# Kernel tuning notes

Hardware: AMD Instinct MI355X
Metric: run time of the kernel (lower is better)

Reference implementation:

```python
import jax, jax.numpy as jnp
import numpy as np

N_NODES = 100000
N_EDGES = 1600000
IN_FEATS = 128
OUT_FEATS = 128
LN_EPS = 1e-5


def setup_inputs() -> dict:
    key = jax.random.key(0)
    k1, k2, k3, k4, k5 = jax.random.split(key, 5)
    h = jax.random.normal(k1, (N_NODES, IN_FEATS), dtype=jnp.float32)
    # nn.Linear(2*in_feats, out_feats): weight [out, 2*in], bias [out]
    stdv = 1.0 / np.sqrt(2 * IN_FEATS)
    W = jax.random.uniform(k2, (OUT_FEATS, 2 * IN_FEATS), dtype=jnp.float32, minval=-stdv, maxval=stdv)
    b = jax.random.uniform(k3, (OUT_FEATS,), dtype=jnp.float32, minval=-stdv, maxval=stdv)
    gamma = jnp.ones((OUT_FEATS,), dtype=jnp.float32)
    beta = jnp.zeros((OUT_FEATS,), dtype=jnp.float32)
    src = jax.random.randint(k4, (N_EDGES,), 0, N_NODES, dtype=jnp.int32)
    dst = jax.random.randint(k5, (N_EDGES,), 0, N_NODES, dtype=jnp.int32)
    return {"h": h, "W": W, "b": b, "gamma": gamma, "beta": beta, "src": src, "dst": dst}


def reference(h, W, b, gamma, beta, src, dst):
    n = h.shape[0]
    ones = jnp.ones(src.shape[0], dtype=h.dtype)
    deg = jax.ops.segment_sum(ones, dst, num_segments=n)          # in-degrees [N]
    norm = jnp.where(deg > 0, 1.0 / deg, 0.0)[:, None]            # inf -> 0
    ah = jax.ops.segment_sum(h[src], dst, num_segments=n)         # copy_src + sum: [N, D]
    cat = jnp.concatenate([h, ah * norm], axis=1)                 # [N, 2D]
    y = cat @ W.T + b                                             # linear -> [N, OUT]
    mu = jnp.mean(y, axis=-1, keepdims=True)
    var = jnp.mean((y - mu) ** 2, axis=-1, keepdims=True)
    y = (y - mu) * jax.lax.rsqrt(var + LN_EPS) * gamma + beta     # LayerNorm
    return jax.nn.relu(y)
```

## Files before the change

kernel.cpp:

```cpp
#include <hip/hip_runtime.h>
#include <hip/hip_bf16.h>

#define LN_EPS 1e-5f

#define NW 4096
#define CHUNK_CAP 96

#define CAP2 1280

#define S_MASK 0x1FFFFu

typedef __attribute__((ext_vector_type(8))) short short8;
typedef __attribute__((ext_vector_type(4))) float f32x4;
typedef __attribute__((ext_vector_type(2))) float f32x2;
typedef __attribute__((ext_vector_type(4))) int int4v;
typedef __attribute__((ext_vector_type(4))) unsigned int uint4v;

#if defined(__has_builtin)
# if __has_builtin(__builtin_amdgcn_cvt_pk_f32_fp8)
#  define HAS_HW_FP8 1
# endif
# if __has_builtin(__builtin_amdgcn_cvt_pk_fp8_f32)
#  define HAS_HW_FP8E 1
# endif
#endif
#ifndef HAS_HW_FP8
# define HAS_HW_FP8 0
#endif
#ifndef HAS_HW_FP8E
# define HAS_HW_FP8E 0
#endif

__device__ __forceinline__ float b2f(unsigned short u) {
    union { unsigned int i; float f; } x; x.i = ((unsigned int)u) << 16; return x.f;
}
__device__ __forceinline__ unsigned short f2b(float f) {
    unsigned int u = __float_as_uint(f);
    unsigned int r = (u + 0x7FFFu + ((u >> 16) & 1u)) >> 16;
    return (unsigned short)r;
}
__device__ __forceinline__ float loadf(const void* p, long long i, int flag) {
    return flag ? ((const float*)p)[i] : b2f(((const unsigned short*)p)[i]);
}

__device__ __forceinline__ unsigned char f2fp8(float x) {
    float ax = fabsf(x);
    unsigned char s = (unsigned char)((__float_as_uint(x) >> 24) & 0x80);
    if (ax >= 448.f) return s | 0x7E;
    if (ax < 0.015625f) {
        int m = (int)(ax * 512.f + 0.5f);
        return s | (unsigned char)m;
    }
    unsigned u = __float_as_uint(ax);
    int e = (int)((u >> 23) & 0xFF) - 127;
    unsigned m = u & 0x7FFFFF;
    unsigned mr = (m + 0x7FFFF + ((m >> 20) & 1)) >> 20;
    unsigned val = (unsigned)((e + 7) << 3) + mr;
    if (val > 0x7E) val = 0x7E;
    return s | (unsigned char)val;
}
__device__ __forceinline__ unsigned enc4(float a, float b, float c, float d) {
#if HAS_HW_FP8E
    int r = __builtin_amdgcn_cvt_pk_fp8_f32(a, b, 0, false);
    r = __builtin_amdgcn_cvt_pk_fp8_f32(c, d, r, true);
    return (unsigned)r;
#else
    return (unsigned)f2fp8(a) | ((unsigned)f2fp8(b) << 8) |
           ((unsigned)f2fp8(c) << 16) | ((unsigned)f2fp8(d) << 24);
#endif
}
__device__ __forceinline__ float fp8d(unsigned v) {
    unsigned s = (v & 0x80) << 24;
    unsigned e = (v >> 3) & 0xF;
    unsigned m = v & 7;
    if (e == 0) {
        float f = (float)m * 0.001953125f;
        return __uint_as_float(s | __float_as_uint(f));
    }
    return __uint_as_float(s | ((e + 120) << 23) | (m << 20));
}
__device__ __forceinline__ void dec16(uint4 u, float* acc) {
#if HAS_HW_FP8
    f32x2 p;
    p = __builtin_amdgcn_cvt_pk_f32_fp8((int)u.x, false); acc[0] += p[0];  acc[1] += p[1];
    p = __builtin_amdgcn_cvt_pk_f32_fp8((int)u.x, true);  acc[2] += p[0];  acc[3] += p[1];
    p = __builtin_amdgcn_cvt_pk_f32_fp8((int)u.y, false); acc[4] += p[0];  acc[5] += p[1];
    p = __builtin_amdgcn_cvt_pk_f32_fp8((int)u.y, true);  acc[6] += p[0];  acc[7] += p[1];
    p = __builtin_amdgcn_cvt_pk_f32_fp8((int)u.z, false); acc[8] += p[0];  acc[9] += p[1];
    p = __builtin_amdgcn_cvt_pk_f32_fp8((int)u.z, true);  acc[10] += p[0]; acc[11] += p[1];
    p = __builtin_amdgcn_cvt_pk_f32_fp8((int)u.w, false); acc[12] += p[0]; acc[13] += p[1];
    p = __builtin_amdgcn_cvt_pk_f32_fp8((int)u.w, true);  acc[14] += p[0]; acc[15] += p[1];
#else
    acc[0] += fp8d(u.x & 0xFF); acc[1] += fp8d((u.x >> 8) & 0xFF);
    acc[2] += fp8d((u.x >> 16) & 0xFF); acc[3] += fp8d(u.x >> 24);
    acc[4] += fp8d(u.y & 0xFF); acc[5] += fp8d((u.y >> 8) & 0xFF);
    acc[6] += fp8d((u.y >> 16) & 0xFF); acc[7] += fp8d(u.y >> 24);
    acc[8] += fp8d(u.z & 0xFF); acc[9] += fp8d((u.z >> 8) & 0xFF);
    acc[10] += fp8d((u.z >> 16) & 0xFF); acc[11] += fp8d(u.z >> 24);
    acc[12] += fp8d(u.w & 0xFF); acc[13] += fp8d((u.w >> 8) & 0xFF);
    acc[14] += fp8d((u.w >> 16) & 0xFF); acc[15] += fp8d(u.w >> 24);
#endif
}

__global__ __launch_bounds__(256) void prep_cvt_kernel(
    const void* __restrict__ h, unsigned char* __restrict__ h8,
    unsigned short* __restrict__ hbf16,
    const void* __restrict__ W, unsigned short* __restrict__ Wbf16,
    int* __restrict__ cnt, int* __restrict__ flag, int n_nodes, int n16) {
    __shared__ int sflag;
    const int tid = threadIdx.x;
    if (tid < 64) {
        const unsigned short* hb = (const unsigned short*)h;
        int bad = 0;
        unsigned short u = hb[2 * tid];        int e = (u >> 7) & 0xFF; bad += (e < 96 || e > 135);
        u = hb[2 * (tid + 64)];                e = (u >> 7) & 0xFF;     bad += (e < 96 || e > 135);
#pragma unroll
        for (int off = 1; off < 64; off <<= 1) bad += __shfl_xor(bad, off);
        if (tid == 0) sflag = (bad > 32) ? 1 : 0;
    }
    __syncthreads();
    const int f = sflag;
    const int idx = blockIdx.x * 256 + tid;
    if (idx < n_nodes) cnt[idx] = 0;
    if (idx == 0) *flag = f;
    if (idx < n16) {
        long long base = (long long)idx * 16;
        uint4 o;
        if (f == 0) {
            const unsigned short* hp = (const unsigned short*)h + base;
            short8 v0 = *(const short8*)hp;
            short8 v1 = *(const short8*)(hp + 8);
            o.x = enc4(b2f((unsigned short)v0[0]), b2f((unsigned short)v0[1]),
                       b2f((unsigned short)v0[2]), b2f((unsigned short)v0[3]));
            o.y = enc4(b2f((unsigned short)v0[4]), b2f((unsigned short)v0[5]),
                       b2f((unsigned short)v0[6]), b2f((unsigned short)v0[7]));
            o.z = enc4(b2f((unsigned short)v1[0]), b2f((unsigned short)v1[1]),
                       b2f((unsigned short)v1[2]), b2f((unsigned short)v1[3]));
            o.w = enc4(b2f((unsigned short)v1[4]), b2f((unsigned short)v1[5]),
                       b2f((unsigned short)v1[6]), b2f((unsigned short)v1[7]));
        } else {
            const float* hf = (const float*)h + base;
            f32x4 a = *(const f32x4*)hf;
            f32x4 b4 = *(const f32x4*)(hf + 4);
            f32x4 c4 = *(const f32x4*)(hf + 8);
            f32x4 d4 = *(const f32x4*)(hf + 12);
            o.x = enc4(a[0], a[1], a[2], a[3]);
            o.y = enc4(b4[0], b4[1], b4[2], b4[3]);
            o.z = enc4(c4[0], c4[1], c4[2], c4[3]);
            o.w = enc4(d4[0], d4[1], d4[2], d4[3]);
            short8 w0, w1;
            w0[0] = (short)f2b(a[0]);  w0[1] = (short)f2b(a[1]);
            w0[2] = (short)f2b(a[2]);  w0[3] = (short)f2b(a[3]);
            w0[4] = (short)f2b(b4[0]); w0[5] = (short)f2b(b4[1]);
            w0[6] = (short)f2b(b4[2]); w0[7] = (short)f2b(b4[3]);
            w1[0] = (short)f2b(c4[0]); w1[1] = (short)f2b(c4[1]);
            w1[2] = (short)f2b(c4[2]); w1[3] = (short)f2b(c4[3]);
            w1[4] = (short)f2b(d4[0]); w1[5] = (short)f2b(d4[1]);
            w1[6] = (short)f2b(d4[2]); w1[7] = (short)f2b(d4[3]);
            __builtin_nontemporal_store(w0, (short8*)&hbf16[base]);
            __builtin_nontemporal_store(w1, (short8*)&hbf16[base + 8]);
        }
        *(uint4*)(h8 + base) = o;
    }
    if (f == 1 && idx < 2048) {
        long long base = (long long)idx * 16;
        const float* wf = (const float*)W + base;
        f32x4 a = *(const f32x4*)wf;
        f32x4 b4 = *(const f32x4*)(wf + 4);
        f32x4 c4 = *(const f32x4*)(wf + 8);
        f32x4 d4 = *(const f32x4*)(wf + 12);
        short8 w0, w1;
        w0[0] = (short)f2b(a[0]);  w0[1] = (short)f2b(a[1]);
        w0[2] = (short)f2b(a[2]);  w0[3] = (short)f2b(a[3]);
        w0[4] = (short)f2b(b4[0]); w0[5] = (short)f2b(b4[1]);
        w0[6] = (short)f2b(b4[2]); w0[7] = (short)f2b(b4[3]);
        w1[0] = (short)f2b(c4[0]); w1[1] = (short)f2b(c4[1]);
        w1[2] = (short)f2b(c4[2]); w1[3] = (short)f2b(c4[3]);
        w1[4] = (short)f2b(d4[0]); w1[5] = (short)f2b(d4[1]);
        w1[6] = (short)f2b(d4[2]); w1[7] = (short)f2b(d4[3]);
        *(short8*)&Wbf16[base] = w0;
        *(short8*)&Wbf16[base + 8] = w1;
    }
}

__global__ __launch_bounds__(256) void bin_kernel(
    const int* __restrict__ src, const int* __restrict__ dst,
    unsigned* __restrict__ bins,
    int* __restrict__ wcnt,
    int n_edges, int part_nodes) {
    const int g = blockIdx.x * 4 + (threadIdx.x >> 6);
    const int lane = threadIdx.x & 63;
    const int epw = (n_edges + NW - 1) / NW;
    const int e0 = g * epw;
    const int e1 = min(e0 + epw, n_edges);
    const unsigned long long below = (1ull << lane) - 1ull;
    const int t4 = part_nodes * 4, t2 = part_nodes * 2;

    int cur0 = 0, cur1 = 0, cur2 = 0, cur3 = 0, cur4 = 0, cur5 = 0, cur6 = 0, cur7 = 0;

    for (int e = e0 + lane;; e += 64) {
        const bool valid = (e < e1);
        if (!__ballot(valid)) break;
        int d = 0, s = 0;
        if (valid) {
            d = __builtin_nontemporal_load(&dst[e]);
            s = __builtin_nontemporal_load(&src[e]);
        }
        int p = 0, dd = d;
        if (dd >= t4) { p += 4; dd -= t4; }
        if (dd >= t2) { p += 2; dd -= t2; }
        if (dd >= part_nodes) { p += 1; dd -= part_nodes; }

        int myoff = CHUNK_CAP;
#pragma unroll
        for (int pp = 0; pp < 8; ++pp) {
            const unsigned long long m = __ballot(valid && (p == pp));
            const int rank = __popcll(m & below);
            const int n = __popcll(m);
            int c = (pp == 0) ? cur0 : (pp == 1) ? cur1 : (pp == 2) ? cur2 :
                    (pp == 3) ? cur3 : (pp == 4) ? cur4 : (pp == 5) ? cur5 :
                    (pp == 6) ? cur6 : cur7;
            if (valid && (p == pp)) myoff = c + rank;
            c += n;
            if (pp == 0) cur0 = c; else if (pp == 1) cur1 = c;
            else if (pp == 2) cur2 = c; else if (pp == 3) cur3 = c;
            else if (pp == 4) cur4 = c; else if (pp == 5) cur5 = c;
            else if (pp == 6) cur6 = c; else cur7 = c;
        }
        if (valid && myoff < CHUNK_CAP) {
            const unsigned pr = ((unsigned)dd << 17) | (unsigned)s;
            bins[((long long)g * 8 + p) * CHUNK_CAP + myoff] = pr;
        }
    }
    int myc = cur0;
    myc = (lane == 1) ? cur1 : myc;  myc = (lane == 2) ? cur2 : myc;
    myc = (lane == 3) ? cur3 : myc;  myc = (lane == 4) ? cur4 : myc;
    myc = (lane == 5) ? cur5 : myc;  myc = (lane == 6) ? cur6 : myc;
    myc = (lane == 7) ? cur7 : myc;
    if (lane < 8) wcnt[g * 8 + lane] = min(myc, CHUNK_CAP);
}

__global__ __launch_bounds__(256) void regroup_kernel(
    const unsigned* __restrict__ bins, const int* __restrict__ wcnt,
    unsigned* __restrict__ bins2, int* __restrict__ gcur,
    int part_nodes) {
    __shared__ int bcnt[256], gbase_s[256], bcur_s[256];
    const int part = blockIdx.x & 7;
    const int rng  = blockIdx.x >> 3;
    const int wbase = rng * 64;
    const int tid = threadIdx.x;
    const int lo = part * part_nodes;
    const int fb_lo = lo >> 6;
    bcnt[tid] = 0;
    __syncthreads();
    const int wv = tid >> 6, lane = tid & 63;
    for (int c = wv; c < 64; c += 4) {
        const int w = wbase + c;
        const int n = wcnt[w * 8 + part];
        const unsigned* cb = bins + ((long long)w * 8 + part) * CHUNK_CAP;
        for (int i = lane; i < n; i += 64) {
            const int node = lo + (int)(cb[i] >> 17);
            atomicAdd(&bcnt[(node >> 6) - fb_lo], 1);
        }
    }
    __syncthreads();
    {
        const int c = bcnt[tid];
        gbase_s[tid] = (c > 0) ? atomicAdd(&gcur[fb_lo + tid], c) : 0;
        bcur_s[tid] = 0;
    }
    __syncthreads();
    for (int c = wv; c < 64; c += 4) {
        const int w = wbase + c;
        const int n = wcnt[w * 8 + part];
        const unsigned* cb = bins + ((long long)w * 8 + part) * CHUNK_CAP;
        for (int i = lane; i < n; i += 64) {
            const unsigned pr = cb[i];
            const int node = lo + (int)(pr >> 17);
            const int lb = (node >> 6) - fb_lo;
            const int r = atomicAdd(&bcur_s[lb], 1);
            const int pos = gbase_s[lb] + r;
            if (pos < CAP2)
                bins2[(long long)(fb_lo + lb) * CAP2 + pos] =
                    ((unsigned)(node & 63) << 17) | (pr & S_MASK);
        }
    }
}

__global__ __launch_bounds__(256) void gather_gemm_ln_kernel(
    const unsigned char* __restrict__ h8,
    const unsigned* __restrict__ bins2,
    const int* __restrict__ gcur,
    const void* __restrict__ h,
    const unsigned short* __restrict__ hbf16,
    const void* __restrict__ W,
    const unsigned short* __restrict__ Wbf16,
    const void* __restrict__ bias,
    const void* __restrict__ gamma,
    const void* __restrict__ beta,
    void* __restrict__ out,
    const int* __restrict__ flagp,
    int n_nodes) {

    __shared__ __align__(16) unsigned short Atile[64 * 264];
    __shared__ __align__(16) char pool[CAP2 * 4];
    __shared__ int ncnt[64], noff[64], ncur[64];
    __shared__ unsigned char perm[64];
    __shared__ float2 mrs[64];

    int* slist = (int*)pool;
    float2* pS = (float2*)pool;

    const int flag = *flagp;
    const int tid = threadIdx.x;
    const int fb = blockIdx.x;
    const int nb0 = fb << 6;

    const unsigned short* hb = flag ? hbf16 : (const unsigned short*)h;
    const unsigned short* Wb = flag ? Wbf16 : (const unsigned short*)W;

#pragma unroll
    for (int j = 0; j < 4; ++j) {
        int u = tid + j * 256;
        int row = u >> 4, seg = u & 15;
        int node = nb0 + row;
        if (node >= n_nodes) node = n_nodes - 1;
        short8 val = __builtin_nontemporal_load(
            (const short8*)(hb + (long long)node * 128 + seg * 8));
        *(short8*)&Atile[row * 264 + seg * 8] = val;
    }

    if (tid < 64) ncnt[tid] = 0;
    __syncthreads();
    const int T = min(gcur[fb], CAP2);
    const unsigned* bb = bins2 + (long long)fb * CAP2;
    for (int i = tid; i < T; i += 256) {
        const int ld = (int)(bb[i] >> 17);
        atomicAdd(&ncnt[ld], 1);
    }
    __syncthreads();
    if (tid < 64) {
        const int mydeg = ncnt[tid];
        int o = 0, rk = 0;
#pragma unroll 1
        for (int j = 0; j < 64; ++j) {
            const int dj = ncnt[j];
            o += (j < tid) ? dj : 0;
            rk += (dj > mydeg) || (dj == mydeg && j < tid);
        }
        noff[tid] = o; ncur[tid] = 0;
        perm[rk] = (unsigned char)tid;
    }
    __syncthreads();
    for (int i = tid; i < T; i += 256) {
        const unsigned pr = bb[i];
        const int ld = (int)(pr >> 17);
        const int r = atomicAdd(&ncur[ld], 1);
        slist[noff[ld] + r] = (int)(pr & S_MASK);
    }
    __syncthreads();

    const int wv = tid >> 6, lane = tid & 63, g = lane >> 3, li = lane & 7;
#pragma unroll 1
    for (int pass = 0; pass < 2; ++pass) {
        const int rank = (pass * 8 + g) * 4 + wv;
        const int ld = perm[rank];
        const int node = nb0 + ld;
        const bool nvalid = (node < n_nodes);
        const int deg = nvalid ? ncnt[ld] : 0;
        const int ofs = noff[ld];
        int mn = deg, mx = deg;
        mn = min(mn, __shfl_xor(mn, 8));  mx = max(mx, __shfl_xor(mx, 8));
        mn = min(mn, __shfl_xor(mn, 16)); mx = max(mx, __shfl_xor(mx, 16));
        mn = min(mn, __shfl_xor(mn, 32)); mx = max(mx, __shfl_xor(mx, 32));

        float acc[16];
#pragma unroll
        for (int j = 0; j < 16; ++j) acc[j] = 0.f;

        int e = 0;
        for (; e + 3 < mn; e += 4) {
            const int s0 = slist[ofs + e];
            const int s1 = slist[ofs + e + 1];
            const int s2 = slist[ofs + e + 2];
            const int s3 = slist[ofs + e + 3];
            uint4 u0 = *(const uint4*)(h8 + (long long)s0 * 128 + li * 16);
            uint4 u1 = *(const uint4*)(h8 + (long long)s1 * 128 + li * 16);
            uint4 u2 = *(const uint4*)(h8 + (long long)s2 * 128 + li * 16);
            uint4 u3 = *(const uint4*)(h8 + (long long)s3 * 128 + li * 16);
            dec16(u0, acc);
            dec16(u1, acc);
            dec16(u2, acc);
            dec16(u3, acc);
        }
        for (; e < mx; ++e) {
            const bool v = (e < deg);
            const int s = slist[min(ofs + (v ? e : 0), CAP2 - 1)];
            uint4 u = *(const uint4*)(h8 + (long long)(v ? s : 0) * 128 + li * 16);
            if (!v) { u.x = 0u; u.y = 0u; u.z = 0u; u.w = 0u; }
            dec16(u, acc);
        }

        const float nrm = deg > 0 ? 1.f / (float)deg : 0.f;
        short8 a0, a1;
        a0[0] = (short)f2b(acc[0] * nrm);  a0[1] = (short)f2b(acc[1] * nrm);
        a0[2] = (short)f2b(acc[2] * nrm);  a0[3] = (short)f2b(acc[3] * nrm);
        a0[4] = (short)f2b(acc[4] * nrm);  a0[5] = (short)f2b(acc[5] * nrm);
        a0[6] = (short)f2b(acc[6] * nrm);  a0[7] = (short)f2b(acc[7] * nrm);
        a1[0] = (short)f2b(acc[8] * nrm);  a1[1] = (short)f2b(acc[9] * nrm);
        a1[2] = (short)f2b(acc[10] * nrm); a1[3] = (short)f2b(acc[11] * nrm);
        a1[4] = (short)f2b(acc[12] * nrm); a1[5] = (short)f2b(acc[13] * nrm);
        a1[6] = (short)f2b(acc[14] * nrm); a1[7] = (short)f2b(acc[15] * nrm);
        *(short8*)&Atile[ld * 264 + 128 + li * 16] = a0;
        *(short8*)&Atile[ld * 264 + 128 + li * 16 + 8] = a1;
    }
    __syncthreads();

    const int q = lane >> 4;
    const int c = lane & 15;

    short8 bfrag[8][2];
#pragma unroll
    for (int ki = 0; ki < 8; ++ki)
#pragma unroll
        for (int t2 = 0; t2 < 2; ++t2)
            bfrag[ki][t2] = *(const short8*)&Wb[(wv * 32 + t2 * 16 + c) * 256 + ki * 32 + q * 8];

    f32x4 acc2[4][2];
#pragma unroll
    for (int rc = 0; rc < 4; ++rc)
#pragma unroll
        for (int t2 = 0; t2 < 2; ++t2) acc2[rc][t2] = (f32x4){0.f, 0.f, 0.f, 0.f};

#pragma unroll
    for (int ki = 0; ki < 8; ++ki) {
        const int kk = ki * 32 + q * 8;
#pragma unroll
        for (int rc = 0; rc < 4; ++rc) {
            const short8 a = *(const short8*)&Atile[(rc * 16 + c) * 264 + kk];
            acc2[rc][0] = __builtin_amdgcn_mfma_f32_16x16x32_bf16(a, bfrag[ki][0], acc2[rc][0], 0, 0, 0);
            acc2[rc][1] = __builtin_amdgcn_mfma_f32_16x16x32_bf16(a, bfrag[ki][1], acc2[rc][1], 0, 0, 0);
        }
    }

    float bcol[2], gcol[2], ecol[2];
#pragma unroll
    for (int t2 = 0; t2 < 2; ++t2) {
        int col = wv * 32 + t2 * 16 + c;
        bcol[t2] = loadf(bias, col, flag);
        gcol[t2] = loadf(gamma, col, flag);
        ecol[t2] = loadf(beta, col, flag);
    }

#pragma unroll
    for (int rc = 0; rc < 4; ++rc)
#pragma unroll
        for (int r = 0; r < 4; ++r) {
            float v0 = acc2[rc][0][r] + bcol[0];
            float v1 = acc2[rc][1][r] + bcol[1];
            float s = v0 + v1;
            float ss = v0 * v0 + v1 * v1;
            s += __shfl_xor(s, 1);  ss += __shfl_xor(ss, 1);
            s += __shfl_xor(s, 2);  ss += __shfl_xor(ss, 2);
            s += __shfl_xor(s, 4);  ss += __shfl_xor(ss, 4);
            s += __shfl_xor(s, 8);  ss += __shfl_xor(ss, 8);
            if (c == 0) {
                int row = rc * 16 + q * 4 + r;
                pS[row * 5 + wv] = make_float2(s, ss);
            }
        }
    __syncthreads();

    if (tid < 64) {
        float s = 0.f, ss = 0.f;
#pragma unroll
        for (int j = 0; j < 4; ++j) {
            float2 p = pS[tid * 5 + j];
            s += p.x; ss += p.y;
        }
        float mean = s * (1.f / 128.f);
        float var = ss * (1.f / 128.f) - mean * mean;
        mrs[tid] = make_float2(mean, rsqrtf(var + LN_EPS));
    }
    __syncthreads();

    if (flag == 0) {
        unsigned short* ostage = Atile;
#pragma unroll
        for (int rc = 0; rc < 4; ++rc)
#pragma unroll
            for (int r = 0; r < 4; ++r) {
                int row = rc * 16 + q * 4 + r;
                float2 m = mrs[row];
#pragma unroll
                for (int t2 = 0; t2 < 2; ++t2) {
                    float o = (acc2[rc][t2][r] + bcol[t2] - m.x) * m.y * gcol[t2] + ecol[t2];
                    o = o > 0.f ? o : 0.f;
                    ostage[row * 128 + wv * 32 + t2 * 16 + c] = f2b(o);
                }
            }
        __syncthreads();
        const uint4v* sv = (const uint4v*)Atile;
#pragma unroll
        for (int rdx = 0; rdx < 4; ++rdx) {
            int u = rdx * 256 + tid;
            int row = u >> 4;
            int node = nb0 + row;
            if (node < n_nodes)
                __builtin_nontemporal_store(sv[u],
                    (uint4v*)((unsigned short*)out + (long long)node * 128 + (u & 15) * 8));
        }
    } else {
        float* ostage = (float*)Atile;
#pragma unroll
        for (int rc = 0; rc < 4; ++rc)
#pragma unroll
            for (int r = 0; r < 4; ++r) {
                int row = rc * 16 + q * 4 + r;
                float2 m = mrs[row];
#pragma unroll
                for (int t2 = 0; t2 < 2; ++t2) {
                    float o = (acc2[rc][t2][r] + bcol[t2] - m.x) * m.y * gcol[t2] + ecol[t2];
                    o = o > 0.f ? o : 0.f;
                    ostage[row * 128 + wv * 32 + t2 * 16 + c] = o;
                }
            }
        __syncthreads();
        const uint4v* sv = (const uint4v*)Atile;
#pragma unroll
        for (int rdx = 0; rdx < 8; ++rdx) {
            int u = rdx * 256 + tid;
            int row = u >> 5;
            int node = nb0 + row;
            if (node < n_nodes)
                __builtin_nontemporal_store(sv[u],
                    (uint4v*)((float*)out + (long long)node * 128 + (u & 31) * 4));
        }
    }
}

extern "C" void kernel_launch(void* const* d_in, const int* in_sizes, int n_in,
                              void* d_out, int out_size, void* d_ws, size_t ws_size,
                              hipStream_t stream) {
    const void* h     = d_in[0];
    const void* W     = d_in[1];
    const void* b     = d_in[2];
    const void* gamma = d_in[3];
    const void* beta  = d_in[4];
    const int* src = (const int*)d_in[5];
    const int* dst = (const int*)d_in[6];

    const int n_nodes = in_sizes[0] / 128;
    const int n_edges = in_sizes[5];
    const int part_nodes = (n_nodes + 7) / 8;
    const int nbuckets = (n_nodes + 63) >> 6;

    char* wsb = (char*)d_ws;
    unsigned short* hbf16 = (unsigned short*)wsb;
    unsigned* bins2 = (unsigned*)(wsb + (size_t)n_nodes * 256);
    unsigned short* Wbf16 = (unsigned short*)((char*)bins2 + (size_t)nbuckets * CAP2 * 4);
    unsigned* bins = (unsigned*)((char*)Wbf16 + 65536);
    int* wcnt = (int*)((char*)bins + (size_t)NW * 8 * CHUNK_CAP * 4);
    int* gcur = (int*)(wsb + (size_t)n_nodes * 512);
    int* flag = gcur + n_nodes;
    unsigned char* h8 = (unsigned char*)(flag + 64);

    int n16 = n_nodes * 8;
    int pgrid = (max(n16, n_nodes) + 255) / 256;
    prep_cvt_kernel<<<pgrid, 256, 0, stream>>>(h, h8, hbf16, W, Wbf16,
                                               gcur, flag, n_nodes, n16);

    bin_kernel<<<NW / 4, 256, 0, stream>>>(src, dst, bins, wcnt, n_edges, part_nodes);

    regroup_kernel<<<512, 256, 0, stream>>>(bins, wcnt, bins2, gcur, part_nodes);

    gather_gemm_ln_kernel<<<nbuckets, 256, 0, stream>>>(h8, bins2, gcur, h, hbf16,
                                                        W, Wbf16, b, gamma, beta,
                                                        d_out, flag, n_nodes);
}
```

Before: 228.4 us.

## Merge prep and bin kernels, stage regroup chunks in LDS, register-cache bucket pairs

```diff
diff --git a/kernel.cpp b/kernel.cpp
--- a/kernel.cpp
+++ b/kernel.cpp
@@ -102,13 +102,71 @@
 #endif
 }
 
-__global__ __launch_bounds__(256) void prep_cvt_kernel(
+__global__ __launch_bounds__(256) void prep_bin_kernel(
     const void* __restrict__ h, unsigned char* __restrict__ h8,
     unsigned short* __restrict__ hbf16,
     const void* __restrict__ W, unsigned short* __restrict__ Wbf16,
-    int* __restrict__ cnt, int* __restrict__ flag, int n_nodes, int n16) {
+    int* __restrict__ cnt, int* __restrict__ flag,
+    const int* __restrict__ src, const int* __restrict__ dst,
+    unsigned* __restrict__ bins, int* __restrict__ wcnt,
+    int n_nodes, int n16, int n_edges, int part_nodes, int nbin_blocks) {
     __shared__ int sflag;
     const int tid = threadIdx.x;
+
+    if ((int)blockIdx.x < nbin_blocks) {
+        const int g = blockIdx.x * 4 + (tid >> 6);
+        const int lane = tid & 63;
+        const int epw = (n_edges + NW - 1) / NW;
+        const int e0 = g * epw;
+        const int e1 = min(e0 + epw, n_edges);
+        const unsigned long long below = (1ull << lane) - 1ull;
+        const int t4 = part_nodes * 4, t2 = part_nodes * 2;
+
+        int cur0 = 0, cur1 = 0, cur2 = 0, cur3 = 0, cur4 = 0, cur5 = 0, cur6 = 0, cur7 = 0;
+
+        for (int e = e0 + lane;; e += 64) {
+            const bool valid = (e < e1);
+            if (!__ballot(valid)) break;
+            int d = 0, s = 0;
+            if (valid) {
+                d = __builtin_nontemporal_load(&dst[e]);
+                s = __builtin_nontemporal_load(&src[e]);
+            }
+            int p = 0, dd = d;
+            if (dd >= t4) { p += 4; dd -= t4; }
+            if (dd >= t2) { p += 2; dd -= t2; }
+            if (dd >= part_nodes) { p += 1; dd -= part_nodes; }
+
+            int myoff = CHUNK_CAP;
+#pragma unroll
+            for (int pp = 0; pp < 8; ++pp) {
+                const unsigned long long m = __ballot(valid && (p == pp));
+                const int rank = __popcll(m & below);
+                const int n = __popcll(m);
+                int c = (pp == 0) ? cur0 : (pp == 1) ? cur1 : (pp == 2) ? cur2 :
+                        (pp == 3) ? cur3 : (pp == 4) ? cur4 : (pp == 5) ? cur5 :
+                        (pp == 6) ? cur6 : cur7;
+                if (valid && (p == pp)) myoff = c + rank;
+                c += n;
+                if (pp == 0) cur0 = c; else if (pp == 1) cur1 = c;
+                else if (pp == 2) cur2 = c; else if (pp == 3) cur3 = c;
+                else if (pp == 4) cur4 = c; else if (pp == 5) cur5 = c;
+                else if (pp == 6) cur6 = c; else cur7 = c;
+            }
+            if (valid && myoff < CHUNK_CAP) {
+                const unsigned pr = ((unsigned)dd << 17) | (unsigned)s;
+                bins[((long long)g * 8 + p) * CHUNK_CAP + myoff] = pr;
+            }
+        }
+        int myc = cur0;
+        myc = (lane == 1) ? cur1 : myc;  myc = (lane == 2) ? cur2 : myc;
+        myc = (lane == 3) ? cur3 : myc;  myc = (lane == 4) ? cur4 : myc;
+        myc = (lane == 5) ? cur5 : myc;  myc = (lane == 6) ? cur6 : myc;
+        myc = (lane == 7) ? cur7 : myc;
+        if (lane < 8) wcnt[g * 8 + lane] = min(myc, CHUNK_CAP);
+        return;
+    }
+
     if (tid < 64) {
         const unsigned short* hb = (const unsigned short*)h;
         int bad = 0;
@@ -120,7 +178,7 @@
     }
     __syncthreads();
     const int f = sflag;
-    const int idx = blockIdx.x * 256 + tid;
+    const int idx = (blockIdx.x - nbin_blocks) * 256 + tid;
     if (idx < n_nodes) cnt[idx] = 0;
     if (idx == 0) *flag = f;
     if (idx < n16) {
@@ -183,67 +241,12 @@
     }
 }
 
-__global__ __launch_bounds__(256) void bin_kernel(
-    const int* __restrict__ src, const int* __restrict__ dst,
-    unsigned* __restrict__ bins,
-    int* __restrict__ wcnt,
-    int n_edges, int part_nodes) {
-    const int g = blockIdx.x * 4 + (threadIdx.x >> 6);
-    const int lane = threadIdx.x & 63;
-    const int epw = (n_edges + NW - 1) / NW;
-    const int e0 = g * epw;
-    const int e1 = min(e0 + epw, n_edges);
-    const unsigned long long below = (1ull << lane) - 1ull;
-    const int t4 = part_nodes * 4, t2 = part_nodes * 2;
-
-    int cur0 = 0, cur1 = 0, cur2 = 0, cur3 = 0, cur4 = 0, cur5 = 0, cur6 = 0, cur7 = 0;
-
-    for (int e = e0 + lane;; e += 64) {
-        const bool valid = (e < e1);
-        if (!__ballot(valid)) break;
-        int d = 0, s = 0;
-        if (valid) {
-            d = __builtin_nontemporal_load(&dst[e]);
-            s = __builtin_nontemporal_load(&src[e]);
-        }
-        int p = 0, dd = d;
-        if (dd >= t4) { p += 4; dd -= t4; }
-        if (dd >= t2) { p += 2; dd -= t2; }
-        if (dd >= part_nodes) { p += 1; dd -= part_nodes; }
-
-        int myoff = CHUNK_CAP;
-#pragma unroll
-        for (int pp = 0; pp < 8; ++pp) {
-            const unsigned long long m = __ballot(valid && (p == pp));
-            const int rank = __popcll(m & below);
-            const int n = __popcll(m);
-            int c = (pp == 0) ? cur0 : (pp == 1) ? cur1 : (pp == 2) ? cur2 :
-                    (pp == 3) ? cur3 : (pp == 4) ? cur4 : (pp == 5) ? cur5 :
-                    (pp == 6) ? cur6 : cur7;
-            if (valid && (p == pp)) myoff = c + rank;
-            c += n;
-            if (pp == 0) cur0 = c; else if (pp == 1) cur1 = c;
-            else if (pp == 2) cur2 = c; else if (pp == 3) cur3 = c;
-            else if (pp == 4) cur4 = c; else if (pp == 5) cur5 = c;
-            else if (pp == 6) cur6 = c; else cur7 = c;
-        }
-        if (valid && myoff < CHUNK_CAP) {
-            const unsigned pr = ((unsigned)dd << 17) | (unsigned)s;
-            bins[((long long)g * 8 + p) * CHUNK_CAP + myoff] = pr;
-        }
-    }
-    int myc = cur0;
-    myc = (lane == 1) ? cur1 : myc;  myc = (lane == 2) ? cur2 : myc;
-    myc = (lane == 3) ? cur3 : myc;  myc = (lane == 4) ? cur4 : myc;
-    myc = (lane == 5) ? cur5 : myc;  myc = (lane == 6) ? cur6 : myc;
-    myc = (lane == 7) ? cur7 : myc;
-    if (lane < 8) wcnt[g * 8 + lane] = min(myc, CHUNK_CAP);
-}
-
 __global__ __launch_bounds__(256) void regroup_kernel(
     const unsigned* __restrict__ bins, const int* __restrict__ wcnt,
     unsigned* __restrict__ bins2, int* __restrict__ gcur,
     int part_nodes) {
+    __shared__ unsigned cpair[64 * CHUNK_CAP];
+    __shared__ int wcnt_s[64];
     __shared__ int bcnt[256], gbase_s[256], bcur_s[256];
     const int part = blockIdx.x & 7;
     const int rng  = blockIdx.x >> 3;
@@ -252,14 +255,20 @@
     const int lo = part * part_nodes;
     const int fb_lo = lo >> 6;
     bcnt[tid] = 0;
-    __syncthreads();
     const int wv = tid >> 6, lane = tid & 63;
     for (int c = wv; c < 64; c += 4) {
         const int w = wbase + c;
         const int n = wcnt[w * 8 + part];
+        if (lane == 0) wcnt_s[c] = n;
         const unsigned* cb = bins + ((long long)w * 8 + part) * CHUNK_CAP;
+        for (int i = lane; i < n; i += 64)
+            cpair[c * CHUNK_CAP + i] = __builtin_nontemporal_load(&cb[i]);
+    }
+    __syncthreads();
+    for (int c = wv; c < 64; c += 4) {
+        const int n = wcnt_s[c];
         for (int i = lane; i < n; i += 64) {
-            const int node = lo + (int)(cb[i] >> 17);
+            const int node = lo + (int)(cpair[c * CHUNK_CAP + i] >> 17);
             atomicAdd(&bcnt[(node >> 6) - fb_lo], 1);
         }
     }
@@ -271,11 +280,9 @@
     }
     __syncthreads();
     for (int c = wv; c < 64; c += 4) {
-        const int w = wbase + c;
-        const int n = wcnt[w * 8 + part];
-        const unsigned* cb = bins + ((long long)w * 8 + part) * CHUNK_CAP;
+        const int n = wcnt_s[c];
         for (int i = lane; i < n; i += 64) {
-            const unsigned pr = cb[i];
+            const unsigned pr = cpair[c * CHUNK_CAP + i];
             const int node = lo + (int)(pr >> 17);
             const int lb = (node >> 6) - fb_lo;
             const int r = atomicAdd(&bcur_s[lb], 1);
@@ -334,9 +341,19 @@
     __syncthreads();
     const int T = min(gcur[fb], CAP2);
     const unsigned* bb = bins2 + (long long)fb * CAP2;
-    for (int i = tid; i < T; i += 256) {
-        const int ld = (int)(bb[i] >> 17);
-        atomicAdd(&ncnt[ld], 1);
+    unsigned pr0 = 0, pr1 = 0, pr2 = 0, pr3 = 0, pr4 = 0;
+    {
+        int i0 = tid, i1 = tid + 256, i2 = tid + 512, i3 = tid + 768, i4 = tid + 1024;
+        if (i0 < T) pr0 = bb[i0];
+        if (i1 < T) pr1 = bb[i1];
+        if (i2 < T) pr2 = bb[i2];
+        if (i3 < T) pr3 = bb[i3];
+        if (i4 < T) pr4 = bb[i4];
+        if (i0 < T) atomicAdd(&ncnt[pr0 >> 17], 1);
+        if (i1 < T) atomicAdd(&ncnt[pr1 >> 17], 1);
+        if (i2 < T) atomicAdd(&ncnt[pr2 >> 17], 1);
+        if (i3 < T) atomicAdd(&ncnt[pr3 >> 17], 1);
+        if (i4 < T) atomicAdd(&ncnt[pr4 >> 17], 1);
     }
     __syncthreads();
     if (tid < 64) {
@@ -352,11 +369,13 @@
         perm[rk] = (unsigned char)tid;
     }
     __syncthreads();
-    for (int i = tid; i < T; i += 256) {
-        const unsigned pr = bb[i];
-        const int ld = (int)(pr >> 17);
-        const int r = atomicAdd(&ncur[ld], 1);
-        slist[noff[ld] + r] = (int)(pr & S_MASK);
+    {
+        int i0 = tid, i1 = tid + 256, i2 = tid + 512, i3 = tid + 768, i4 = tid + 1024;
+        if (i0 < T) { int ld = (int)(pr0 >> 17); slist[noff[ld] + atomicAdd(&ncur[ld], 1)] = (int)(pr0 & S_MASK); }
+        if (i1 < T) { int ld = (int)(pr1 >> 17); slist[noff[ld] + atomicAdd(&ncur[ld], 1)] = (int)(pr1 & S_MASK); }
+        if (i2 < T) { int ld = (int)(pr2 >> 17); slist[noff[ld] + atomicAdd(&ncur[ld], 1)] = (int)(pr2 & S_MASK); }
+        if (i3 < T) { int ld = (int)(pr3 >> 17); slist[noff[ld] + atomicAdd(&ncur[ld], 1)] = (int)(pr3 & S_MASK); }
+        if (i4 < T) { int ld = (int)(pr4 >> 17); slist[noff[ld] + atomicAdd(&ncur[ld], 1)] = (int)(pr4 & S_MASK); }
     }
     __syncthreads();
 
@@ -567,10 +586,12 @@
 
     int n16 = n_nodes * 8;
     int pgrid = (max(n16, n_nodes) + 255) / 256;
-    prep_cvt_kernel<<<pgrid, 256, 0, stream>>>(h, h8, hbf16, W, Wbf16,
-                                               gcur, flag, n_nodes, n16);
-
-    bin_kernel<<<NW / 4, 256, 0, stream>>>(src, dst, bins, wcnt, n_edges, part_nodes);
+    const int nbin_blocks = NW / 4;
+
+    prep_bin_kernel<<<nbin_blocks + pgrid, 256, 0, stream>>>(
+        h, h8, hbf16, W, Wbf16, gcur, flag,
+        src, dst, bins, wcnt,
+        n_nodes, n16, n_edges, part_nodes, nbin_blocks);
 
     regroup_kernel<<<512, 256, 0, stream>>>(bins, wcnt, bins2, gcur, part_nodes);
 
```

After: 221.0 us. -3.2%, faster.
